# Kernel tuning notes

Measured on AMD Instinct MI355X. Metric: run time of the kernel, lower is better.

Reference implementation:

```python
import jax, jax.numpy as jnp
import numpy as np

D = 64
NEG = 0.01            # leakyrelu_neg_slope
X_CONN = 0.25         # x_connection_init
SKIP_H = 0.5          # skip_weight_h
SIGMAS = np.asarray(1.5 ** np.arange(15), np.float32)  # all_sigmas_dist

N_LIG, N_REC = 4096, 8192
E_LIG, E_REC = 65536, 262144
F_LIG, F_REC, NRBF = 15, 27, 15


def _lrelu(x):
    return jax.nn.leaky_relu(x, NEG)


def _ln(x, g, b, eps=1e-5):
    m = x.mean(-1, keepdims=True)
    v = ((x - m) ** 2).mean(-1, keepdims=True)
    return (x - m) * jax.lax.rsqrt(v + eps) * g + b


def _mlp2(x, w1, b1, g, bt, w2, b2):
    # nn.Sequential(Linear, Dropout(0), LeakyReLU, LayerNorm, Linear) in eval mode
    return _ln(_lrelu(x @ w1 + b1), g, bt) @ w2 + b2


def _coords_mlp(m, w1, b1, w2, b2):
    # nn.Sequential(Linear, Dropout(0), LeakyReLU, Linear(out,1))
    return _lrelu(m @ w1 + b1) @ w2 + b2  # [E, 1]


def _seg_mean(v, idx, n):
    # DGL fn.mean over incoming edges at destination nodes (0 for isolated nodes)
    s = jax.ops.segment_sum(v, idx, num_segments=n)
    c = jax.ops.segment_sum(jnp.ones(idx.shape, v.dtype), idx, num_segments=n)
    return s / jnp.maximum(c, 1.0)[:, None]


def setup_inputs() -> dict:
    key = jax.random.key(0)
    ks = iter(jax.random.split(key, 64))

    def n(shape, s=1.0):
        return jax.random.normal(next(ks), shape, jnp.float32) * s

    def lin(i, o):
        return n((i, o), 1.0 / float(np.sqrt(i)))

    zeros = lambda *s: jnp.zeros(s, jnp.float32)
    ones = lambda *s: jnp.ones(s, jnp.float32)

    d = {}
    d['coords_lig'] = n((N_LIG, 3))
    d['h_lig'] = n((N_LIG, D))
    d['orig_h_lig'] = n((N_LIG, D))
    d['orig_coords_lig'] = n((N_LIG, 3))
    d['coords_rec'] = n((N_REC, 3))
    d['h_rec'] = n((N_REC, D))
    d['orig_h_rec'] = n((N_REC, D))
    d['orig_coords_rec'] = n((N_REC, 3))
    d['lig_src'] = jax.random.randint(next(ks), (E_LIG,), 0, N_LIG)
    d['lig_dst'] = jax.random.randint(next(ks), (E_LIG,), 0, N_LIG)
    d['lig_efeat'] = n((E_LIG, F_LIG))
    d['rec_src'] = jax.random.randint(next(ks), (E_REC,), 0, N_REC)
    d['rec_dst'] = jax.random.randint(next(ks), (E_REC,), 0, N_REC)
    d['rec_efeat'] = n((E_REC, F_REC))
    d['mask'] = (jax.random.uniform(next(ks), (N_LIG, N_REC)) < 0.5).astype(jnp.float32)
    # ---- parameters ----
    d['lig_em_w1'], d['lig_em_b1'] = lin(2 * D + F_LIG + NRBF, D), zeros(D)
    d['lig_em_g'], d['lig_em_bt'] = ones(D), zeros(D)
    d['lig_em_w2'], d['lig_em_b2'] = lin(D, D), zeros(D)
    d['rec_em_w1'], d['rec_em_b1'] = lin(2 * D + F_REC + NRBF, D), zeros(D)
    d['rec_em_g'], d['rec_em_bt'] = ones(D), zeros(D)
    d['rec_em_w2'], d['rec_em_b2'] = lin(D, D), zeros(D)
    d['lig_cm_w1'], d['lig_cm_b1'] = lin(D, D), zeros(D)
    d['lig_cm_w2'], d['lig_cm_b2'] = lin(D, 1), zeros(1)
    d['rec_cm_w1'], d['rec_cm_b1'] = lin(D, D), zeros(D)
    d['rec_cm_w2'], d['rec_cm_b2'] = lin(D, 1), zeros(1)
    for nm in ['q_lig_w', 'k_lig_w', 'v_lig_w', 'q_rec_w', 'k_rec_w', 'v_rec_w']:
        d[nm] = lin(D, D)
    d['lig_nm_w1'], d['lig_nm_b1'] = lin(4 * D, D), zeros(D)
    d['lig_nm_g'], d['lig_nm_bt'] = ones(D), zeros(D)
    d['lig_nm_w2'], d['lig_nm_b2'] = lin(D, D), zeros(D)
    d['rec_nm_w1'], d['rec_nm_b1'] = lin(4 * D, D), zeros(D)
    d['rec_nm_g'], d['rec_nm_bt'] = ones(D), zeros(D)
    d['rec_nm_w2'], d['rec_nm_b2'] = lin(D, D), zeros(D)
    return d


def reference(coords_lig, h_lig, orig_h_lig, orig_coords_lig,
              coords_rec, h_rec, orig_h_rec, orig_coords_rec,
              lig_src, lig_dst, lig_efeat, rec_src, rec_dst, rec_efeat, mask,
              lig_em_w1, lig_em_b1, lig_em_g, lig_em_bt, lig_em_w2, lig_em_b2,
              rec_em_w1, rec_em_b1, rec_em_g, rec_em_bt, rec_em_w2, rec_em_b2,
              lig_cm_w1, lig_cm_b1, lig_cm_w2, lig_cm_b2,
              rec_cm_w1, rec_cm_b1, rec_cm_w2, rec_cm_b2,
              q_lig_w, k_lig_w, v_lig_w, q_rec_w, k_rec_w, v_rec_w,
              lig_nm_w1, lig_nm_b1, lig_nm_g, lig_nm_bt, lig_nm_w2, lig_nm_b2,
              rec_nm_w1, rec_nm_b1, rec_nm_g, rec_nm_bt, rec_nm_w2, rec_nm_b2):
    n_lig, n_rec = coords_lig.shape[0], coords_rec.shape[0]
    sig = jnp.asarray(SIGMAS, coords_lig.dtype)

    # --- ligand edge messages: x_rel = x_src - x_dst, multi-scale RBF of |x_rel|^2 ---
    xr_l = coords_lig[lig_src] - coords_lig[lig_dst]                       # [E_l, 3]
    rbf_l = jnp.exp(-jnp.sum(xr_l * xr_l, -1, keepdims=True) / sig)        # [E_l, 15]
    msg_l = _mlp2(jnp.concatenate([h_lig[lig_src], h_lig[lig_dst], lig_efeat, rbf_l], -1),
                  lig_em_w1, lig_em_b1, lig_em_g, lig_em_bt, lig_em_w2, lig_em_b2)

    # --- receptor edge messages (rec_square_distance_scale = 1) ---
    xr_r = coords_rec[rec_src] - coords_rec[rec_dst]
    rbf_r = jnp.exp(-jnp.sum(xr_r * xr_r, -1, keepdims=True) / sig)
    msg_r = _mlp2(jnp.concatenate([h_rec[rec_src], h_rec[rec_dst], rec_efeat, rbf_r], -1),
                  rec_em_w1, rec_em_b1, rec_em_g, rec_em_bt, rec_em_w2, rec_em_b2)

    # --- masked cross-graph attention (pre/post cross-msg norms are identity) ---
    q_l, k_l, v_l = _lrelu(h_lig @ q_lig_w), _lrelu(h_lig @ k_lig_w), h_lig @ v_lig_w
    q_r, k_r, v_r = _lrelu(h_rec @ q_rec_w), _lrelu(h_rec @ k_rec_w), h_rec @ v_rec_w
    s_lr = mask * (q_l @ k_r.T) - 1000.0 * (1.0 - mask)
    att_l = jax.nn.softmax(s_lr, axis=1) @ v_r                             # [N_l, D]
    mt = mask.T
    s_rl = mt * (q_r @ k_l.T) - 1000.0 * (1.0 - mt)
    att_r = jax.nn.softmax(s_rl, axis=1) @ v_l                             # [N_r, D]

    # --- equivariant coordinate update: mean_j phi_x(m_ij) * x_rel, + skip to orig ---
    coef_l = _coords_mlp(msg_l, lig_cm_w1, lig_cm_b1, lig_cm_w2, lig_cm_b2)
    x_lig = X_CONN * orig_coords_lig + (1.0 - X_CONN) * coords_lig + _seg_mean(xr_l * coef_l, lig_dst, n_lig)
    coef_r = _coords_mlp(msg_r, rec_cm_w1, rec_cm_b1, rec_cm_w2, rec_cm_b2)
    x_rec = X_CONN * orig_coords_rec + (1.0 - X_CONN) * coords_rec + _seg_mean(xr_r * coef_r, rec_dst, n_rec)

    # --- node feature update with skip (h_feats_dim == out_feats_dim) ---
    aggr_l = _seg_mean(msg_l, lig_dst, n_lig)
    h_lig_out = SKIP_H * _mlp2(jnp.concatenate([h_lig, aggr_l, att_l, orig_h_lig], -1),
                               lig_nm_w1, lig_nm_b1, lig_nm_g, lig_nm_bt, lig_nm_w2, lig_nm_b2) \
        + (1.0 - SKIP_H) * h_lig
    aggr_r = _seg_mean(msg_r, rec_dst, n_rec)
    h_rec_out = SKIP_H * _mlp2(jnp.concatenate([h_rec, aggr_r, att_r, orig_h_rec], -1),
                               rec_nm_w1, rec_nm_b1, rec_nm_g, rec_nm_bt, rec_nm_w2, rec_nm_b2) \
        + (1.0 - SKIP_H) * h_rec
    return x_lig, h_lig_out, x_rec, h_rec_out
```

## Files before the change

### kernel.cpp

```cpp
#include <hip/hip_runtime.h>
#include <hip/hip_bf16.h>

typedef __hip_bfloat16 bf16;
typedef __attribute__((ext_vector_type(8))) short bfrag8;
typedef __attribute__((ext_vector_type(4))) float f32x4;

#define N_LIG 4096
#define N_REC 8192
#define E_LIG 65536
#define E_REC 262144
#define F_LIGc 15
#define F_RECc 27

__device__ __forceinline__ float ldkv(const float* p, size_t i) { return p[i]; }
__device__ __forceinline__ float ldkv(const bf16* p, size_t i) { return __bfloat162float(p[i]); }
__device__ __forceinline__ short bfbits(float x) {
    bf16 b = __float2bfloat16(x);
    return *(short*)&b;
}
__device__ __forceinline__ unsigned short stg(const float* p, size_t i) {
    return (unsigned short)bfbits(p[i]);
}
__device__ __forceinline__ unsigned short stg(const bf16* p, size_t i) {
    return *(const unsigned short*)(p + i);
}
__device__ __forceinline__ void stage16(unsigned short* d, const bf16* s) {
    *(uint4*)d = *(const uint4*)s;
}
__device__ __forceinline__ void stage16(unsigned short* d, const float* s) {
    float4 a = *(const float4*)s;
    float4 b = *(const float4*)(s + 4);
    unsigned short tmp[8] = {
        (unsigned short)bfbits(a.x), (unsigned short)bfbits(a.y),
        (unsigned short)bfbits(a.z), (unsigned short)bfbits(a.w),
        (unsigned short)bfbits(b.x), (unsigned short)bfbits(b.y),
        (unsigned short)bfbits(b.z), (unsigned short)bfbits(b.w)};
    *(uint4*)d = *(uint4*)tmp;
}

__device__ __forceinline__ int swz(int row, int col) {
    return (row << 6) + ((((col >> 3) ^ row ^ (row >> 3)) & 7) << 3) + (col & 7);
}

__constant__ float c_inv_sigma[15] = {
    1.0f, 0.6666666667f, 0.4444444444f, 0.2962962963f, 0.1975308642f,
    0.1316872428f, 0.08779149520f, 0.05852766346f, 0.03901844231f,
    0.02601229487f, 0.01734152992f, 0.01156101994f, 0.007707346628f,
    0.005138231085f, 0.003425487390f};

__device__ __forceinline__ float wave_sum(float v) {
    #pragma unroll
    for (int o = 32; o > 0; o >>= 1) v += __shfl_xor(v, o, 64);
    return v;
}
__device__ __forceinline__ float quad_max(float v) {
    v = fmaxf(v, __shfl_xor(v, 1)); v = fmaxf(v, __shfl_xor(v, 2));
    v = fmaxf(v, __shfl_xor(v, 4)); v = fmaxf(v, __shfl_xor(v, 8));
    return v;
}

__device__ __forceinline__ void pack_body(
    int b, int t,
    const float* w_rec1, const float* w_lig1, const float* w_rec2, const float* w_lig2,
    const float* c_rec1, const float* c_lig1,
    unsigned short* p_rec1, unsigned short* p_lig1,
    unsigned short* p_rec2, unsigned short* p_lig2,
    unsigned short* pc_rec1, unsigned short* pc_lig1)
{
    const float* src; unsigned short* dst; int kk, IN;
    if (b < 6)       { src = w_rec1; dst = p_rec1;  kk = b;      IN = 170; }
    else if (b < 11) { src = w_lig1; dst = p_lig1;  kk = b - 6;  IN = 158; }
    else if (b < 13) { src = w_rec2; dst = p_rec2;  kk = b - 11; IN = 64; }
    else if (b < 15) { src = w_lig2; dst = p_lig2;  kk = b - 13; IN = 64; }
    else if (b < 17) { src = c_rec1; dst = pc_rec1; kk = b - 15; IN = 64; }
    else             { src = c_lig1; dst = pc_lig1; kk = b - 17; IN = 64; }
    int wv = t >> 6, L = t & 63, lm = L & 15, qd = L >> 4;
    int n = wv * 16 + lm;
    unsigned short tmp[8];
    #pragma unroll
    for (int j = 0; j < 8; ++j) {
        int k = kk * 32 + qd * 8 + j;
        tmp[j] = (k < IN) ? (unsigned short)bfbits(src[k * 64 + n]) : (unsigned short)0;
    }
    *(uint4*)&dst[((size_t)(kk * 4 + wv) * 64 + L) * 8] = *(uint4*)tmp;
}

__device__ __forceinline__ void kv_body(
    int job, int j,
    const float* h_lig, const float* h_rec,
    const float* kwl, const float* vwl, const float* kwr, const float* vwr,
    bf16* kbl, bf16* vbl, bf16* kbr, bf16* vbr)
{
    const float *h, *w; bf16* out; int node, do_l;
    if (job < N_LIG)                  { h = h_lig; w = kwl; out = kbl; node = job;                     do_l = 1; }
    else if (job < 2 * N_LIG)         { h = h_lig; w = vwl; out = vbl; node = job - N_LIG;             do_l = 0; }
    else if (job < 2 * N_LIG + N_REC) { h = h_rec; w = kwr; out = kbr; node = job - 2 * N_LIG;         do_l = 1; }
    else                              { h = h_rec; w = vwr; out = vbr; node = job - 2 * N_LIG - N_REC; do_l = 0; }
    float xv = h[(size_t)node * 64 + j];
    float acc = 0.f;
    #pragma unroll
    for (int i = 0; i < 64; ++i) acc += __shfl(xv, i, 64) * w[i * 64 + j];
    if (do_l) acc = acc > 0.f ? acc : 0.01f * acc;
    out[(size_t)node * 64 + j] = __float2bfloat16(acc);
}

__device__ __forceinline__ void mask_body(
    unsigned char* tr, unsigned char* tc, int bx, int by, int t,
    const float* mask, unsigned long long* mq, unsigned long long* mqT, int R, int C)
{
    int r0 = by * 64, c0 = bx * 64;
    int cs = (t & 15) * 4;
    #pragma unroll
    for (int rr = 0; rr < 4; ++rr) {
        int r = (t >> 4) + rr * 16;
        const float* mp = &mask[(size_t)(r0 + r) * C + c0 + cs];
        unsigned char b0 = mp[0] != 0.f, b1 = mp[1] != 0.f;
        unsigned char b2 = mp[2] != 0.f, b3 = mp[3] != 0.f;
        tr[r * 68 + cs + 0] = b0; tr[r * 68 + cs + 1] = b1;
        tr[r * 68 + cs + 2] = b2; tr[r * 68 + cs + 3] = b3;
        tc[(cs + 0) * 68 + r] = b0; tc[(cs + 1) * 68 + r] = b1;
        tc[(cs + 2) * 68 + r] = b2; tc[(cs + 3) * 68 + r] = b3;
    }
    __syncthreads();
    if (t < 128) {
        const unsigned* p = (t < 64) ? (const unsigned*)&tr[t * 68]
                                     : (const unsigned*)&tc[(t - 64) * 68];
        unsigned lo = 0, hi = 0;
        #pragma unroll
        for (int i = 0; i < 8; ++i)
            lo |= (((p[i] & 0x01010101u) * 0x01020408u) >> 24 & 0xFu) << (4 * i);
        #pragma unroll
        for (int i = 8; i < 16; ++i)
            hi |= (((p[i] & 0x01010101u) * 0x01020408u) >> 24 & 0xFu) << (4 * (i - 8));
        unsigned long long w = (unsigned long long)lo | ((unsigned long long)hi << 32);
        if (t < 64) mq[(size_t)(c0 >> 6) * R + r0 + t] = w;
        else        mqT[(size_t)(r0 >> 6) * C + c0 + (t - 64)] = w;
    }
}

#define NB_MASK  ((N_REC / 64) * (N_LIG / 64))
#define N_CVT    (N_LIG * 64 + N_REC * 64 + E_LIG * F_LIGc + E_REC * F_RECc)
#define NB_CVT   (N_CVT / 256)
#define NB_KV    (2 * (N_LIG + N_REC) / 4)
#define N_ZERO   (N_LIG * 64 + N_REC * 64 + N_LIG * 3 + N_REC * 3 + N_LIG + N_REC)
#define NB_HIST  ((E_LIG + E_REC) / 256)
#define NB_PACK  19
#define NB_PREP  (NB_MASK + NB_CVT + NB_KV + NB_HIST + NB_PACK)

__global__ __launch_bounds__(256) void prep_kernel(
    const float* __restrict__ mask, unsigned long long* __restrict__ mq,
    unsigned long long* __restrict__ mqT,
    const float* __restrict__ h_lig, bf16* __restrict__ hb_l,
    const float* __restrict__ h_rec, bf16* __restrict__ hb_r,
    const float* __restrict__ ef_l, bf16* __restrict__ efb_l,
    const float* __restrict__ ef_r, bf16* __restrict__ efb_r,
    const float* __restrict__ kwl, const float* __restrict__ vwl,
    const float* __restrict__ kwr, const float* __restrict__ vwr,
    bf16* __restrict__ kbl, bf16* __restrict__ vbl,
    bf16* __restrict__ kbr, bf16* __restrict__ vbr,
    const int* __restrict__ dl, const int* __restrict__ dr,
    int* __restrict__ cl, int* __restrict__ cr,
    const float* w_rec1, const float* w_lig1, const float* w_rec2, const float* w_lig2,
    const float* c_rec1, const float* c_lig1,
    unsigned short* p_rec1, unsigned short* p_lig1,
    unsigned short* p_rec2, unsigned short* p_lig2,
    unsigned short* pc_rec1, unsigned short* pc_lig1)
{
    __shared__ unsigned char tr[64 * 68];
    __shared__ unsigned char tc[64 * 68];
    int b = blockIdx.x, t = threadIdx.x;
    if (b < NB_MASK) {
        mask_body(tr, tc, b & 127, b >> 7, t, mask, mq, mqT, N_LIG, N_REC);
        return;
    }
    b -= NB_MASK;
    if (b < NB_CVT) {
        int i = b * 256 + t;
        if (i < N_LIG * 64) { hb_l[i] = __float2bfloat16(h_lig[i]); return; }
        i -= N_LIG * 64;
        if (i < N_REC * 64) { hb_r[i] = __float2bfloat16(h_rec[i]); return; }
        i -= N_REC * 64;
        if (i < E_LIG * F_LIGc) { efb_l[i] = __float2bfloat16(ef_l[i]); return; }
        i -= E_LIG * F_LIGc;
        efb_r[i] = __float2bfloat16(ef_r[i]);
        return;
    }
    b -= NB_CVT;
    if (b < NB_KV) {
        kv_body(b * 4 + (t >> 6), t & 63, h_lig, h_rec, kwl, vwl, kwr, vwr,
                kbl, vbl, kbr, vbr);
        return;
    }
    b -= NB_KV;
    if (b < NB_HIST) {
        int i = b * 256 + t;
        if (i < E_LIG) atomicAdd(&cl[dl[i]], 1);
        else atomicAdd(&cr[dr[i - E_LIG]], 1);
        return;
    }
    b -= NB_HIST;
    pack_body(b, t, w_rec1, w_lig1, w_rec2, w_lig2, c_rec1, c_lig1,
              p_rec1, p_lig1, p_rec2, p_lig2, pc_rec1, pc_lig1);
}

__global__ void zero_kernel(float* __restrict__ p, int n) {
    int i = blockIdx.x * blockDim.x + threadIdx.x;
    if (i < n) p[i] = 0.f;
}
__global__ void hist2_kernel(const int* __restrict__ dl, const int* __restrict__ dr,
                             int* __restrict__ cl, int* __restrict__ cr) {
    int i = blockIdx.x * 256 + threadIdx.x;
    if (i < E_LIG) { atomicAdd(&cl[dl[i]], 1); return; }
    i -= E_LIG;
    if (i < E_REC) atomicAdd(&cr[dr[i]], 1);
}
__global__ __launch_bounds__(256) void pack_frags(
    const float* w_rec1, const float* w_lig1, const float* w_rec2, const float* w_lig2,
    const float* c_rec1, const float* c_lig1,
    unsigned short* p_rec1, unsigned short* p_lig1,
    unsigned short* p_rec2, unsigned short* p_lig2,
    unsigned short* pc_rec1, unsigned short* pc_lig1)
{
    pack_body(blockIdx.x, threadIdx.x, w_rec1, w_lig1, w_rec2, w_lig2, c_rec1, c_lig1,
              p_rec1, p_lig1, p_rec2, p_lig2, pc_rec1, pc_lig1);
}
__global__ __launch_bounds__(256) void kv_proj_kernel(
    const float* __restrict__ h_lig, const float* __restrict__ h_rec,
    const float* __restrict__ kwl, const float* __restrict__ vwl,
    const float* __restrict__ kwr, const float* __restrict__ vwr,
    bf16* __restrict__ kbl, bf16* __restrict__ vbl,
    bf16* __restrict__ kbr, bf16* __restrict__ vbr)
{
    kv_body(blockIdx.x * 4 + (threadIdx.x >> 6), threadIdx.x & 63,
            h_lig, h_rec, kwl, vwl, kwr, vwr, kbl, vbl, kbr, vbr);
}

__global__ __launch_bounds__(256) void scan2_kernel(
    const int* __restrict__ cl, int* __restrict__ curl,
    const int* __restrict__ cr, int* __restrict__ curr)
{
    const int* counts = blockIdx.x ? cr : cl;
    int* cursor = blockIdx.x ? curr : curl;
    int n = blockIdx.x ? N_REC : N_LIG;
    __shared__ int part[256];
    int t = threadIdx.x;
    int c = n / 256;
    int base = t * c;
    int s = 0;
    for (int i = 0; i < c; ++i) s += counts[base + i];
    part[t] = s;
    __syncthreads();
    for (int o = 1; o < 256; o <<= 1) {
        int u = (t >= o) ? part[t - o] : 0;
        __syncthreads();
        part[t] += u;
        __syncthreads();
    }
    int run = part[t] - s;
    for (int i = 0; i < c; ++i) {
        cursor[base + i] = run;
        run += counts[base + i];
    }
}

__global__ void scatter2_kernel(const int* __restrict__ dl, const int* __restrict__ dr,
                                int* __restrict__ curl, int* __restrict__ curr,
                                int* __restrict__ ordl, int* __restrict__ ordr) {
    int i = blockIdx.x * 256 + threadIdx.x;
    if (i < E_LIG) { ordl[atomicAdd(&curl[dl[i]], 1)] = i; return; }
    i -= E_LIG;
    if (i < E_REC) ordr[atomicAdd(&curr[dr[i]], 1)] = i;
}

template <int F, int K1S, typename HT>
__device__ __forceinline__ void edge_body(
    char* sbuf, int ebid,
    const int* __restrict__ order,
    const float* __restrict__ coords, const HT* __restrict__ h,
    const int* __restrict__ src, const int* __restrict__ dst,
    const HT* __restrict__ efeat,
    const unsigned short* __restrict__ w1p, const float* __restrict__ b1,
    const float* __restrict__ g, const float* __restrict__ bt,
    const unsigned short* __restrict__ w2p, const float* __restrict__ b2,
    const unsigned short* __restrict__ c1p, const float* __restrict__ cb1,
    const float* __restrict__ cw2, const float* __restrict__ cb2,
    float* __restrict__ aggr, float* __restrict__ xacc)
{
    constexpr int IN = 143 + F;
    constexpr int KP = K1S * 32 + 8;
    constexpr int XB = 64 * KP * 2;
    static_assert(XB >= 64 * 68 * 4, "msgf f32 alias must fit in xb");
    static_assert(XB >= 64 * 72 * 2, "h1b alias must fit in xb");
    unsigned short* xb   = (unsigned short*)sbuf;
    unsigned short* h1b  = (unsigned short*)sbuf;
    float*          msgf = (float*)sbuf;
    float* wsum1   = (float*)(sbuf + XB);
    float* wsum2   = (float*)(sbuf + XB + 1024);
    float* stat_m  = (float*)(sbuf + XB + 2048);
    float* stat_r  = (float*)(sbuf + XB + 2304);
    float* coefp   = (float*)(sbuf + XB + 2560);
    float* coef_all= (float*)(sbuf + XB + 3584);
    int*   srcs    = (int*)(sbuf + XB + 3840);
    int*   dsts    = (int*)(sbuf + XB + 4096);
    int*   ords    = (int*)(sbuf + XB + 4352);
    float* xr_s    = (float*)(sbuf + XB + 4608);
    float* d2s     = (float*)(sbuf + XB + 5376);

// ... 406 lines not shown
        #pragma unroll
        for (int r = 0; r < 4; ++r) {
            int row = r0 + wv * 16 + qd * 4 + r;
            pM[(size_t)sp * n_rows + row] = rm[r];
            pL[(size_t)sp * n_rows + row] = osum[r];
        }
    }
}

__global__ __launch_bounds__(256, 4) void mega_kernel(
    int nb1,
    const float* h1, const float* qw1, const bf16* k1, const bf16* v1,
    const unsigned long long* mq1, float* pO1, float* pM1, float* pL1,
    int nrows1, int ncols1, int ns1,
    const float* h2, const float* qw2, const bf16* k2, const bf16* v2,
    const unsigned long long* mq2, float* pO2, float* pM2, float* pL2,
    int nrows2, int ncols2, int ns2,
    const int* ordR, const float* coordsR, const bf16* hR,
    const int* srcR, const int* dstR, const bf16* efR,
    const unsigned short* w1pR, const float* b1R, const float* gR, const float* btR,
    const unsigned short* w2pR, const float* b2R,
    const unsigned short* c1pR, const float* cb1R, const float* cw2R, const float* cb2R,
    float* aggrR, float* xaccR,
    const int* ordL, const float* coordsL, const bf16* hL,
    const int* srcL, const int* dstL, const bf16* efL,
    const unsigned short* w1pL, const float* b1L, const float* gL, const float* btL,
    const unsigned short* w2pL, const float* b2L,
    const unsigned short* c1pL, const float* cb1L, const float* cw2L, const float* cb2L,
    float* aggrL, float* xaccL)
{
    __shared__ __align__(16) char sbuf[31232];
    int bid = blockIdx.x;
    const int nbAtt = (N_LIG / 64) * ns1 + (N_REC / 64) * ns2;
    if (bid < nbAtt) {
        attn_body<0>(sbuf, bid, nb1,
            h1, qw1, k1, v1, mq1, (const float*)0, 0L, 0L, pO1, pM1, pL1, nrows1, ncols1, ns1,
            h2, qw2, k2, v2, mq2, (const float*)0, 0L, 0L, pO2, pM2, pL2, nrows2, ncols2, ns2);
    } else {
        int eid = bid - nbAtt;
        if (eid < E_REC / 64)
            edge_body<F_RECc, 6, bf16>(sbuf, eid, ordR, coordsR, hR, srcR, dstR, efR,
                w1pR, b1R, gR, btR, w2pR, b2R, c1pR, cb1R, cw2R, cb2R, aggrR, xaccR);
        else
            edge_body<F_LIGc, 5, bf16>(sbuf, eid - E_REC / 64, ordL, coordsL, hL, srcL, dstL, efL,
                w1pL, b1L, gL, btL, w2pL, b2L, c1pL, cb1L, cw2L, cb2L, aggrL, xaccL);
    }
}

template <int F, int K1S>
__global__ __launch_bounds__(256, 4) void edge_mfma_f(
    const int* order, const float* coords, const float* h,
    const int* src, const int* dst, const float* efeat,
    const unsigned short* w1p, const float* b1, const float* g, const float* bt,
    const unsigned short* w2p, const float* b2,
    const unsigned short* c1p, const float* cb1, const float* cw2, const float* cb2,
    float* aggr, float* xacc)
{
    __shared__ __align__(16) char sbuf[64 * (K1S * 32 + 8) * 2 + 5632];
    edge_body<F, K1S, float>(sbuf, blockIdx.x, order, coords, h, src, dst, efeat,
        w1p, b1, g, bt, w2p, b2, c1p, cb1, cw2, cb2, aggr, xacc);
}

__global__ __launch_bounds__(256, 4) void attn_f32mask(
    int nb1,
    const float* h1, const float* qw1, const bf16* k1, const bf16* v1,
    const float* mf1, long mrs1, long mcs1,
    float* pO1, float* pM1, float* pL1, int nrows1, int ncols1, int ns1,
    const float* h2, const float* qw2, const bf16* k2, const bf16* v2,
    const float* mf2, long mrs2, long mcs2,
    float* pO2, float* pM2, float* pL2, int nrows2, int ncols2, int ns2)
{
    __shared__ __align__(16) char sbuf[29696];
    attn_body<1>(sbuf, blockIdx.x, nb1,
        h1, qw1, k1, v1, (const unsigned long long*)0, mf1, mrs1, mcs1,
        pO1, pM1, pL1, nrows1, ncols1, ns1,
        h2, qw2, k2, v2, (const unsigned long long*)0, mf2, mrs2, mcs2,
        pO2, pM2, pL2, nrows2, ncols2, ns2);
}

__global__ __launch_bounds__(256, 3) void node_mfma(
    int nbl, int nbn,
    const float* h1, const float* __restrict__ aggr1, const int* __restrict__ cnt1,
    const float* att1, const float* __restrict__ origh1,
    const float* __restrict__ w1a, const float* __restrict__ b1a,
    const float* __restrict__ ga, const float* __restrict__ bta,
    const float* __restrict__ w2a, const float* __restrict__ b2a, float* out1,
    const float* h2, const float* __restrict__ aggr2, const int* __restrict__ cnt2,
    const float* att2, const float* __restrict__ origh2,
    const float* __restrict__ w1b, const float* __restrict__ b1b,
    const float* __restrict__ gb, const float* __restrict__ btb,
    const float* __restrict__ w2b, const float* __restrict__ b2b, float* out2,
    const float* __restrict__ ocl, const float* __restrict__ ccl,
    const float* __restrict__ xaccl, float* __restrict__ outxl,
    const float* __restrict__ ocr, const float* __restrict__ ccr,
    const float* __restrict__ xaccr, float* __restrict__ outxr)
{
    if ((int)blockIdx.x >= nbn) {
        int i = (blockIdx.x - nbn) * 256 + threadIdx.x;
        if (i < N_LIG * 3) {
            int node = i / 3;
            float invc = 1.f / fmaxf((float)cnt1[node], 1.f);
            outxl[i] = 0.25f * ocl[i] + 0.75f * ccl[i] + xaccl[i] * invc;
        } else {
            i -= N_LIG * 3;
            if (i < N_REC * 3) {
                int node = i / 3;
                float invc = 1.f / fmaxf((float)cnt2[node], 1.f);
                outxr[i] = 0.25f * ocr[i] + 0.75f * ccr[i] + xaccr[i] * invc;
            }
        }
        return;
    }

    const float *h, *aggr, *att, *orig_h, *w1, *b1, *g, *bt, *w2, *b2;
    const int* cnt;
    float* h_out;
    int n0;
    if ((int)blockIdx.x < nbl) {
        h = h1; aggr = aggr1; cnt = cnt1; att = att1; orig_h = origh1;
        w1 = w1a; b1 = b1a; g = ga; bt = bta; w2 = w2a; b2 = b2a; h_out = out1;
        n0 = blockIdx.x * 64;
    } else {
        h = h2; aggr = aggr2; cnt = cnt2; att = att2; orig_h = origh2;
        w1 = w1b; b1 = b1b; g = gb; bt = btb; w2 = w2b; b2 = b2b; h_out = out2;
        n0 = (blockIdx.x - nbl) * 64;
    }

    constexpr int KP = 264;
    __shared__ __align__(16) char smem[64 * KP * 2];
    __shared__ __align__(16) unsigned short h1b[64 * 72];
    __shared__ float sums[256], sums2[256];
    __shared__ float stat_m[64], stat_r[64];
    unsigned short* xb  = (unsigned short*)smem;
    float*          h1f = (float*)smem;

    const int t  = threadIdx.x;
    const int lm = t & 15;
    const int qd = (t & 63) >> 4;
    const int n  = (t >> 6) * 16 + lm;

    bfrag8 w1f[8], w2f[2];
    #pragma unroll
    for (int kk = 0; kk < 8; ++kk)
        #pragma unroll
        for (int j = 0; j < 8; ++j) {
            int k = kk * 32 + qd * 8 + j;
            w1f[kk][j] = bfbits(w1[k * 64 + n]);
        }
    #pragma unroll
    for (int kk = 0; kk < 2; ++kk)
        #pragma unroll
        for (int j = 0; j < 8; ++j) {
            int k = kk * 32 + qd * 8 + j;
            w2f[kk][j] = bfbits(w2[k * 64 + n]);
        }
    const float b1n = b1[n], b2n = b2[n];

    for (int p = 0; p < 16; ++p) {
        int e = (t >> 6) + 4 * p;
        int node = n0 + e;
        float invc = 1.f / fmaxf((float)cnt[node], 1.f);
        int j = t & 63;
        xb[e * KP + j]       = bfbits(h[(size_t)node * 64 + j]);
        xb[e * KP + 64 + j]  = bfbits(aggr[(size_t)node * 64 + j] * invc);
        xb[e * KP + 128 + j] = bfbits(att[(size_t)node * 64 + j]);
        xb[e * KP + 192 + j] = bfbits(orig_h[(size_t)node * 64 + j]);
    }
    __syncthreads();

    f32x4 acc1[4];
    #pragma unroll
    for (int m = 0; m < 4; ++m) {
        f32x4 acc = {0.f, 0.f, 0.f, 0.f};
        #pragma unroll
        for (int kk = 0; kk < 8; ++kk) {
            bfrag8 a = *(const bfrag8*)&xb[(m * 16 + lm) * KP + kk * 32 + qd * 8];
            acc = __builtin_amdgcn_mfma_f32_16x16x32_bf16(a, w1f[kk], acc, 0, 0, 0);
        }
        acc1[m] = acc;
    }
    __syncthreads();
    #pragma unroll
    for (int m = 0; m < 4; ++m)
        #pragma unroll
        for (int r = 0; r < 4; ++r) {
            int mr = m * 16 + qd * 4 + r;
            float v = acc1[m][r] + b1n;
            v = v > 0.f ? v : 0.01f * v;
            h1f[mr * 68 + n] = v;
        }
    __syncthreads();

    {
        int e = t >> 2, seg = (t & 3) * 16;
        float s1 = 0.f, s2 = 0.f;
        #pragma unroll
        for (int j = 0; j < 16; ++j) {
            float v = h1f[e * 68 + seg + j];
            s1 += v; s2 += v * v;
        }
        sums[t] = s1; sums2[t] = s2;
    }
    __syncthreads();
    if (t < 64) {
        float s1 = sums[4 * t] + sums[4 * t + 1] + sums[4 * t + 2] + sums[4 * t + 3];
        float s2 = sums2[4 * t] + sums2[4 * t + 1] + sums2[4 * t + 2] + sums2[4 * t + 3];
        float mean = s1 * (1.f / 64.f);
        float var = s2 * (1.f / 64.f) - mean * mean;
        stat_m[t] = mean;
        stat_r[t] = rsqrtf(fmaxf(var, 0.f) + 1e-5f);
    }
    __syncthreads();
    for (int idx = t; idx < 4096; idx += 256) {
        int e = idx >> 6, j = idx & 63;
        float v = (h1f[e * 68 + j] - stat_m[e]) * stat_r[e] * g[j] + bt[j];
        h1b[e * 72 + j] = bfbits(v);
    }
    __syncthreads();

    #pragma unroll
    for (int m = 0; m < 4; ++m) {
        f32x4 acc = {0.f, 0.f, 0.f, 0.f};
        #pragma unroll
        for (int kk = 0; kk < 2; ++kk) {
            bfrag8 a = *(const bfrag8*)&h1b[(m * 16 + lm) * 72 + kk * 32 + qd * 8];
            acc = __builtin_amdgcn_mfma_f32_16x16x32_bf16(a, w2f[kk], acc, 0, 0, 0);
        }
        #pragma unroll
        for (int r = 0; r < 4; ++r) {
            int row = n0 + m * 16 + qd * 4 + r;
            float o = acc[r] + b2n;
            float hv = h[(size_t)row * 64 + n];
            h_out[(size_t)row * 64 + n] = 0.5f * o + 0.5f * hv;
        }
    }
}

__global__ __launch_bounds__(64) void attn_merge2(
    const float* __restrict__ pO1, const float* __restrict__ pM1, const float* __restrict__ pL1,
    float* __restrict__ out1, int ns1,
    const float* __restrict__ pO2, const float* __restrict__ pM2, const float* __restrict__ pL2,
    float* __restrict__ out2, int ns2)
{
    int r = blockIdx.x;
    const float *pO, *pM, *pL; float* out; int n_rows, nsplit;
    if (r < N_LIG) { pO = pO1; pM = pM1; pL = pL1; out = out1; n_rows = N_LIG; nsplit = ns1; }
    else { r -= N_LIG; pO = pO2; pM = pM2; pL = pL2; out = out2; n_rows = N_REC; nsplit = ns2; }
    int d = threadIdx.x;
    float mstar = -1e30f;
// ... 47 lines not shown
    int wid = tid >> 6;
    if ((tid & 63) == 0) red[wid] = lmax;
    __syncthreads();
    float bmax = fmaxf(fmaxf(red[0], red[1]), fmaxf(red[2], red[3]));
    __syncthreads();

    float lsum = 0.f;
    for (int c = tid; c < n_cols; c += 256) {
        float e = __expf(sc[c] - bmax);
        sc[c] = e;
        lsum += e;
    }
    lsum = wave_sum(lsum);
    if ((tid & 63) == 0) red[wid] = lsum;
    __syncthreads();
    float inv = 1.f / (red[0] + red[1] + red[2] + red[3]);

    int dd = tid & 63;
    float o = 0.f;
    for (int c = wid; c < n_cols; c += 4) o += sc[c] * ldkv(v, (size_t)c * 64 + dd);
    opart[wid][dd] = o;
    __syncthreads();
    if (wid == 0)
        out[(size_t)row * 64 + dd] =
            (opart[0][dd] + opart[1][dd] + opart[2][dd] + opart[3][dd]) * inv;
}

extern "C" void kernel_launch(void* const* d_in, const int* in_sizes, int n_in,
                              void* d_out, int out_size, void* d_ws, size_t ws_size,
                              hipStream_t stream)
{
    const float* coords_lig      = (const float*)d_in[0];
    const float* h_lig           = (const float*)d_in[1];
    const float* orig_h_lig      = (const float*)d_in[2];
    const float* orig_coords_lig = (const float*)d_in[3];
    const float* coords_rec      = (const float*)d_in[4];
    const float* h_rec           = (const float*)d_in[5];
    const float* orig_h_rec      = (const float*)d_in[6];
    const float* orig_coords_rec = (const float*)d_in[7];
    const int* lig_src   = (const int*)d_in[8];
    const int* lig_dst   = (const int*)d_in[9];
    const float* lig_efeat = (const float*)d_in[10];
    const int* rec_src   = (const int*)d_in[11];
    const int* rec_dst   = (const int*)d_in[12];
    const float* rec_efeat = (const float*)d_in[13];
    const float* mask      = (const float*)d_in[14];
    const float *lig_em_w1 = (const float*)d_in[15], *lig_em_b1 = (const float*)d_in[16];
    const float *lig_em_g  = (const float*)d_in[17], *lig_em_bt = (const float*)d_in[18];
    const float *lig_em_w2 = (const float*)d_in[19], *lig_em_b2 = (const float*)d_in[20];
    const float *rec_em_w1 = (const float*)d_in[21], *rec_em_b1 = (const float*)d_in[22];
    const float *rec_em_g  = (const float*)d_in[23], *rec_em_bt = (const float*)d_in[24];
    const float *rec_em_w2 = (const float*)d_in[25], *rec_em_b2 = (const float*)d_in[26];
    const float *lig_cm_w1 = (const float*)d_in[27], *lig_cm_b1 = (const float*)d_in[28];
    const float *lig_cm_w2 = (const float*)d_in[29], *lig_cm_b2 = (const float*)d_in[30];
    const float *rec_cm_w1 = (const float*)d_in[31], *rec_cm_b1 = (const float*)d_in[32];
    const float *rec_cm_w2 = (const float*)d_in[33], *rec_cm_b2 = (const float*)d_in[34];
    const float *q_lig_w = (const float*)d_in[35], *k_lig_w = (const float*)d_in[36];
    const float *v_lig_w = (const float*)d_in[37], *q_rec_w = (const float*)d_in[38];
    const float *k_rec_w = (const float*)d_in[39], *v_rec_w = (const float*)d_in[40];
    const float *lig_nm_w1 = (const float*)d_in[41], *lig_nm_b1 = (const float*)d_in[42];
    const float *lig_nm_g  = (const float*)d_in[43], *lig_nm_bt = (const float*)d_in[44];
    const float *lig_nm_w2 = (const float*)d_in[45], *lig_nm_b2 = (const float*)d_in[46];
    const float *rec_nm_w1 = (const float*)d_in[47], *rec_nm_b1 = (const float*)d_in[48];
    const float *rec_nm_g  = (const float*)d_in[49], *rec_nm_bt = (const float*)d_in[50];
    const float *rec_nm_w2 = (const float*)d_in[51], *rec_nm_b2 = (const float*)d_in[52];

    char* wsb = (char*)d_ws;
    float* aggr_l = (float*)(wsb + 16);
    float* aggr_r = aggr_l + (size_t)N_LIG * 64;
    float* xacc_l = aggr_r + (size_t)N_REC * 64;
    float* xacc_r = xacc_l + (size_t)N_LIG * 3;
    int* counts_l = (int*)(xacc_r + (size_t)N_REC * 3);
    int* counts_r = counts_l + N_LIG;
    int* cursor_l = counts_r + N_REC;
    int* cursor_r = cursor_l + N_LIG;
    int* order_l  = cursor_r + N_REC;
    int* order_r  = order_l + E_LIG;
    unsigned short* p_rec1  = (unsigned short*)(order_r + E_REC);
    unsigned short* p_lig1  = p_rec1 + 6 * 2048;
    unsigned short* p_rec2  = p_lig1 + 5 * 2048;
    unsigned short* p_lig2  = p_rec2 + 2 * 2048;
    unsigned short* pc_rec1 = p_lig2 + 2 * 2048;
    unsigned short* pc_lig1 = pc_rec1 + 2 * 2048;
    char* kv_base = (char*)(pc_lig1 + 2 * 2048);
    const size_t core_b = (size_t)(kv_base - wsb);
    const size_t kv_b = (size_t)(N_LIG + N_REC) * 64 * 2 * 2;

    const size_t mq1_n = (size_t)(N_REC / 64) * N_LIG;
    const size_t mq2_n = (size_t)(N_LIG / 64) * N_REC;
    const size_t mq_all_b = (mq1_n + mq2_n) * 8;
    const size_t mir_b = (size_t)(N_LIG + N_REC) * 64 * 2
                       + ((size_t)E_LIG * F_LIGc + (size_t)E_REC * F_RECc) * 2;

    const size_t part_b_hi = ((size_t)16 * N_LIG * 64 + (size_t)8 * N_REC * 64) * 4
                           + ((size_t)16 * N_LIG + (size_t)8 * N_REC) * 2 * 4;
    const size_t part_b_lo = ((size_t)4 * N_LIG * 64 + (size_t)2 * N_REC * 64) * 4
                           + ((size_t)4 * N_LIG + (size_t)2 * N_REC) * 2 * 4;

    int tier, ns1, ns2;
    size_t part_b;
    if (ws_size >= core_b + kv_b + part_b_hi + mq_all_b + mir_b) {
        tier = 0; ns1 = 16; ns2 = 8; part_b = part_b_hi;
    } else if (ws_size >= core_b + kv_b + part_b_lo) {
        tier = 1; ns1 = 4; ns2 = 2; part_b = part_b_lo;
    } else {
        tier = 2; ns1 = 4; ns2 = 2; part_b = part_b_lo;
    }

    bf16* kb_l = (bf16*)kv_base;
    bf16* vb_l = kb_l + (size_t)N_LIG * 64;
    bf16* kb_r = vb_l + (size_t)N_LIG * 64;
    bf16* vb_r = kb_r + (size_t)N_REC * 64;
    float* pO1 = (float*)(kv_base + kv_b);
    float* pO2 = pO1 + (size_t)ns1 * N_LIG * 64;
    float* pM1 = pO2 + (size_t)ns2 * N_REC * 64;
    float* pL1 = pM1 + (size_t)ns1 * N_LIG;
    float* pM2 = pL1 + (size_t)ns1 * N_LIG;
    float* pL2 = pM2 + (size_t)ns2 * N_REC;
    unsigned long long* mqb  = (unsigned long long*)(kv_base + kv_b + part_b);
    unsigned long long* mqbT = mqb + mq1_n;
    bf16* hb_l  = (bf16*)(mqbT + mq2_n);
    bf16* hb_r  = hb_l + (size_t)N_LIG * 64;
    bf16* efb_l = hb_r + (size_t)N_REC * 64;
    bf16* efb_r = efb_l + (size_t)E_LIG * F_LIGc;

    float* out = (float*)d_out;
    float* x_lig_o = out;
    float* h_lig_o = out + 12288;
    float* x_rec_o = out + 274432;
    float* h_rec_o = out + 299008;

    const int nb1 = (N_LIG / 64) * ns1;
    const int nb2 = (N_REC / 64) * ns2;

    if (tier == 0) {
        zero_kernel<<<(N_ZERO + 255) / 256, 256, 0, stream>>>(aggr_l, N_ZERO);
        prep_kernel<<<NB_PREP, 256, 0, stream>>>(
            mask, mqb, mqbT,
            h_lig, hb_l, h_rec, hb_r, lig_efeat, efb_l, rec_efeat, efb_r,
            k_lig_w, v_lig_w, k_rec_w, v_rec_w, kb_l, vb_l, kb_r, vb_r,
            lig_dst, rec_dst, counts_l, counts_r,
            rec_em_w1, lig_em_w1, rec_em_w2, lig_em_w2, rec_cm_w1, lig_cm_w1,
            p_rec1, p_lig1, p_rec2, p_lig2, pc_rec1, pc_lig1);
        scan2_kernel<<<2, 256, 0, stream>>>(counts_l, cursor_l, counts_r, cursor_r);
        scatter2_kernel<<<(E_LIG + E_REC) / 256, 256, 0, stream>>>(
            lig_dst, rec_dst, cursor_l, cursor_r, order_l, order_r);

        mega_kernel<<<nb1 + nb2 + (E_LIG + E_REC) / 64, 256, 0, stream>>>(
            nb1,
            h_lig, q_lig_w, kb_r, vb_r, mqb, pO1, pM1, pL1, N_LIG, N_REC, ns1,
            h_rec, q_rec_w, kb_l, vb_l, mqbT, pO2, pM2, pL2, N_REC, N_LIG, ns2,
            order_r, coords_rec, hb_r, rec_src, rec_dst, efb_r,
            p_rec1, rec_em_b1, rec_em_g, rec_em_bt, p_rec2, rec_em_b2,
            pc_rec1, rec_cm_b1, rec_cm_w2, rec_cm_b2, aggr_r, xacc_r,
            order_l, coords_lig, hb_l, lig_src, lig_dst, efb_l,
            p_lig1, lig_em_b1, lig_em_g, lig_em_bt, p_lig2, lig_em_b2,
            pc_lig1, lig_cm_b1, lig_cm_w2, lig_cm_b2, aggr_l, xacc_l);

        attn_merge2<<<N_LIG + N_REC, 64, 0, stream>>>(
            pO1, pM1, pL1, h_lig_o, ns1, pO2, pM2, pL2, h_rec_o, ns2);
    } else {
        zero_kernel<<<(N_ZERO + 255) / 256, 256, 0, stream>>>(aggr_l, N_ZERO);
        pack_frags<<<19, 256, 0, stream>>>(
            rec_em_w1, lig_em_w1, rec_em_w2, lig_em_w2, rec_cm_w1, lig_cm_w1,
            p_rec1, p_lig1, p_rec2, p_lig2, pc_rec1, pc_lig1);
        hist2_kernel<<<(E_LIG + E_REC) / 256, 256, 0, stream>>>(
            lig_dst, rec_dst, counts_l, counts_r);
        scan2_kernel<<<2, 256, 0, stream>>>(counts_l, cursor_l, counts_r, cursor_r);
        scatter2_kernel<<<(E_LIG + E_REC) / 256, 256, 0, stream>>>(
            lig_dst, rec_dst, cursor_l, cursor_r, order_l, order_r);
        kv_proj_kernel<<<(2 * (N_LIG + N_REC)) / 4, 256, 0, stream>>>(
            h_lig, h_rec, k_lig_w, v_lig_w, k_rec_w, v_rec_w,
            kb_l, vb_l, kb_r, vb_r);

        edge_mfma_f<F_LIGc, 5><<<E_LIG / 64, 256, 0, stream>>>(
            order_l, coords_lig, h_lig, lig_src, lig_dst, lig_efeat,
            p_lig1, lig_em_b1, lig_em_g, lig_em_bt, p_lig2, lig_em_b2,
            pc_lig1, lig_cm_b1, lig_cm_w2, lig_cm_b2, aggr_l, xacc_l);
        edge_mfma_f<F_RECc, 6><<<E_REC / 64, 256, 0, stream>>>(
            order_r, coords_rec, h_rec, rec_src, rec_dst, rec_efeat,
            p_rec1, rec_em_b1, rec_em_g, rec_em_bt, p_rec2, rec_em_b2,
            pc_rec1, rec_cm_b1, rec_cm_w2, rec_cm_b2, aggr_r, xacc_r);
        if (tier == 1) {
            attn_f32mask<<<nb1 + nb2, 256, 0, stream>>>(
                nb1,
                h_lig, q_lig_w, kb_r, vb_r, mask, (long)N_REC, 1L,
                pO1, pM1, pL1, N_LIG, N_REC, ns1,
                h_rec, q_rec_w, kb_l, vb_l, mask, 1L, (long)N_REC,
                pO2, pM2, pL2, N_REC, N_LIG, ns2);
            attn_merge2<<<N_LIG + N_REC, 64, 0, stream>>>(
                pO1, pM1, pL1, h_lig_o, ns1, pO2, pM2, pL2, h_rec_o, ns2);
        } else {
            attn_row_kernel<<<N_LIG, 256, N_REC * sizeof(float), stream>>>(
                h_lig, q_lig_w, kb_r, vb_r, mask, (long)N_REC, 1L, h_lig_o, N_REC);
            attn_row_kernel<<<N_REC, 256, N_LIG * sizeof(float), stream>>>(
                h_rec, q_rec_w, kb_l, vb_l, mask, 1L, (long)N_REC, h_rec_o, N_LIG);
        }
    }

    const int nbn = N_LIG / 64 + N_REC / 64;
    const int nbc = ((N_LIG + N_REC) * 3 + 255) / 256;
    node_mfma<<<nbn + nbc, 256, 0, stream>>>(
        N_LIG / 64, nbn,
        h_lig, aggr_l, counts_l, h_lig_o, orig_h_lig,
        lig_nm_w1, lig_nm_b1, lig_nm_g, lig_nm_bt, lig_nm_w2, lig_nm_b2, h_lig_o,
        h_rec, aggr_r, counts_r, h_rec_o, orig_h_rec,
        rec_nm_w1, rec_nm_b1, rec_nm_g, rec_nm_bt, rec_nm_w2, rec_nm_b2, h_rec_o,
        orig_coords_lig, coords_lig, xacc_l, x_lig_o,
        orig_coords_rec, coords_rec, xacc_r, x_rec_o);
}
```

Baseline: 571.5 us.

## Prepack node-MLP weights, vectorize bf16 conversion, fold zeroing into prep kernel

Node-MLP weights are now packed once into MFMA fragment layout in the prep and pack kernels, so node_mfma blocks load fragments with single vector loads instead of gathering scalar fp32 weights in every block. Node-feature staging in node_mfma uses float4 loads with the per-node inverse count held in shared memory. The fp32-to-bf16 conversion handles four elements per thread, and most buffer zeroing moves into prep_kernel blocks so the standalone zero kernel only clears the counts. In exchange the prep launch grows, and the pack stage gains blocks and workspace.

```diff
diff --git a/kernel.cpp b/kernel.cpp
--- a/kernel.cpp
+++ b/kernel.cpp
@@ -37,6 +37,13 @@
         (unsigned short)bfbits(b.z), (unsigned short)bfbits(b.w)};
     *(uint4*)d = *(uint4*)tmp;
 }
+__device__ __forceinline__ void cv4(bf16* d, const float* s) {
+    float4 v = *(const float4*)s;
+    unsigned short tmp[4] = {
+        (unsigned short)bfbits(v.x), (unsigned short)bfbits(v.y),
+        (unsigned short)bfbits(v.z), (unsigned short)bfbits(v.w)};
+    *(uint2*)d = *(uint2*)tmp;
+}
 
 __device__ __forceinline__ int swz(int row, int col) {
     return (row << 6) + ((((col >> 3) ^ row ^ (row >> 3)) & 7) << 3) + (col & 7);
@@ -63,9 +70,12 @@
     int b, int t,
     const float* w_rec1, const float* w_lig1, const float* w_rec2, const float* w_lig2,
     const float* c_rec1, const float* c_lig1,
+    const float* n_rec1, const float* n_lig1, const float* n_rec2, const float* n_lig2,
     unsigned short* p_rec1, unsigned short* p_lig1,
     unsigned short* p_rec2, unsigned short* p_lig2,
-    unsigned short* pc_rec1, unsigned short* pc_lig1)
+    unsigned short* pc_rec1, unsigned short* pc_lig1,
+    unsigned short* pn_rec1, unsigned short* pn_lig1,
+    unsigned short* pn_rec2, unsigned short* pn_lig2)
 {
     const float* src; unsigned short* dst; int kk, IN;
     if (b < 6)       { src = w_rec1; dst = p_rec1;  kk = b;      IN = 170; }
@@ -73,7 +83,11 @@
     else if (b < 13) { src = w_rec2; dst = p_rec2;  kk = b - 11; IN = 64; }
     else if (b < 15) { src = w_lig2; dst = p_lig2;  kk = b - 13; IN = 64; }
     else if (b < 17) { src = c_rec1; dst = pc_rec1; kk = b - 15; IN = 64; }
-    else             { src = c_lig1; dst = pc_lig1; kk = b - 17; IN = 64; }
+    else if (b < 19) { src = c_lig1; dst = pc_lig1; kk = b - 17; IN = 64; }
+    else if (b < 27) { src = n_rec1; dst = pn_rec1; kk = b - 19; IN = 256; }
+    else if (b < 35) { src = n_lig1; dst = pn_lig1; kk = b - 27; IN = 256; }
+    else if (b < 37) { src = n_rec2; dst = pn_rec2; kk = b - 35; IN = 64; }
+    else             { src = n_lig2; dst = pn_lig2; kk = b - 37; IN = 64; }
     int wv = t >> 6, L = t & 63, lm = L & 15, qd = L >> 4;
     int n = wv * 16 + lm;
     unsigned short tmp[8];
@@ -138,14 +152,16 @@
     }
 }
 
-#define NB_MASK  ((N_REC / 64) * (N_LIG / 64))
-#define N_CVT    (N_LIG * 64 + N_REC * 64 + E_LIG * F_LIGc + E_REC * F_RECc)
-#define NB_CVT   (N_CVT / 256)
-#define NB_KV    (2 * (N_LIG + N_REC) / 4)
-#define N_ZERO   (N_LIG * 64 + N_REC * 64 + N_LIG * 3 + N_REC * 3 + N_LIG + N_REC)
-#define NB_HIST  ((E_LIG + E_REC) / 256)
-#define NB_PACK  19
-#define NB_PREP  (NB_MASK + NB_CVT + NB_KV + NB_HIST + NB_PACK)
+#define NB_MASK   ((N_REC / 64) * (N_LIG / 64))
+#define N_CVT     (N_LIG * 64 + N_REC * 64 + E_LIG * F_LIGc + E_REC * F_RECc)
+#define NB_CVT4   (N_CVT / 1024)
+#define NB_KV     (2 * (N_LIG + N_REC) / 4)
+#define N_ZEROA   (N_LIG * 64 + N_REC * 64 + N_LIG * 3 + N_REC * 3)
+#define NB_ZEROA  (N_ZEROA / 256)
+#define N_ZERO    (N_ZEROA + N_LIG + N_REC)
+#define NB_HIST   ((E_LIG + E_REC) / 256)
+#define NB_PACK   39
+#define NB_PREP   (NB_MASK + NB_CVT4 + NB_KV + NB_ZEROA + NB_HIST + NB_PACK)
 
 __global__ __launch_bounds__(256) void prep_kernel(
     const float* __restrict__ mask, unsigned long long* __restrict__ mq,
@@ -158,13 +174,17 @@
     const float* __restrict__ kwr, const float* __restrict__ vwr,
     bf16* __restrict__ kbl, bf16* __restrict__ vbl,
     bf16* __restrict__ kbr, bf16* __restrict__ vbr,
+    float* __restrict__ zp,
     const int* __restrict__ dl, const int* __restrict__ dr,
     int* __restrict__ cl, int* __restrict__ cr,
     const float* w_rec1, const float* w_lig1, const float* w_rec2, const float* w_lig2,
     const float* c_rec1, const float* c_lig1,
+    const float* n_rec1, const float* n_lig1, const float* n_rec2, const float* n_lig2,
     unsigned short* p_rec1, unsigned short* p_lig1,
     unsigned short* p_rec2, unsigned short* p_lig2,
-    unsigned short* pc_rec1, unsigned short* pc_lig1)
+    unsigned short* pc_rec1, unsigned short* pc_lig1,
+    unsigned short* pn_rec1, unsigned short* pn_lig1,
+    unsigned short* pn_rec2, unsigned short* pn_lig2)
 {
     __shared__ unsigned char tr[64 * 68];
     __shared__ unsigned char tc[64 * 68];
@@ -174,24 +194,29 @@
         return;
     }
     b -= NB_MASK;
-    if (b < NB_CVT) {
-        int i = b * 256 + t;
-        if (i < N_LIG * 64) { hb_l[i] = __float2bfloat16(h_lig[i]); return; }
+    if (b < NB_CVT4) {
+        int i = (b * 256 + t) * 4;
+        if (i < N_LIG * 64) { cv4(hb_l + i, h_lig + i); return; }
         i -= N_LIG * 64;
-        if (i < N_REC * 64) { hb_r[i] = __float2bfloat16(h_rec[i]); return; }
+        if (i < N_REC * 64) { cv4(hb_r + i, h_rec + i); return; }
         i -= N_REC * 64;
-        if (i < E_LIG * F_LIGc) { efb_l[i] = __float2bfloat16(ef_l[i]); return; }
+        if (i < E_LIG * F_LIGc) { cv4(efb_l + i, ef_l + i); return; }
         i -= E_LIG * F_LIGc;
-        efb_r[i] = __float2bfloat16(ef_r[i]);
+        cv4(efb_r + i, ef_r + i);
         return;
     }
-    b -= NB_CVT;
+    b -= NB_CVT4;
     if (b < NB_KV) {
         kv_body(b * 4 + (t >> 6), t & 63, h_lig, h_rec, kwl, vwl, kwr, vwr,
                 kbl, vbl, kbr, vbr);
         return;
     }
     b -= NB_KV;
+    if (b < NB_ZEROA) {
+        zp[b * 256 + t] = 0.f;
+        return;
+    }
+    b -= NB_ZEROA;
     if (b < NB_HIST) {
         int i = b * 256 + t;
         if (i < E_LIG) atomicAdd(&cl[dl[i]], 1);
@@ -200,7 +225,9 @@
     }
     b -= NB_HIST;
     pack_body(b, t, w_rec1, w_lig1, w_rec2, w_lig2, c_rec1, c_lig1,
-              p_rec1, p_lig1, p_rec2, p_lig2, pc_rec1, pc_lig1);
+              n_rec1, n_lig1, n_rec2, n_lig2,
+              p_rec1, p_lig1, p_rec2, p_lig2, pc_rec1, pc_lig1,
+              pn_rec1, pn_lig1, pn_rec2, pn_lig2);
 }
 
 __global__ void zero_kernel(float* __restrict__ p, int n) {
@@ -217,12 +244,17 @@
 __global__ __launch_bounds__(256) void pack_frags(
     const float* w_rec1, const float* w_lig1, const float* w_rec2, const float* w_lig2,
     const float* c_rec1, const float* c_lig1,
+    const float* n_rec1, const float* n_lig1, const float* n_rec2, const float* n_lig2,
     unsigned short* p_rec1, unsigned short* p_lig1,
     unsigned short* p_rec2, unsigned short* p_lig2,
-    unsigned short* pc_rec1, unsigned short* pc_lig1)
+    unsigned short* pc_rec1, unsigned short* pc_lig1,
+    unsigned short* pn_rec1, unsigned short* pn_lig1,
+    unsigned short* pn_rec2, unsigned short* pn_lig2)
 {
     pack_body(blockIdx.x, threadIdx.x, w_rec1, w_lig1, w_rec2, w_lig2, c_rec1, c_lig1,
-              p_rec1, p_lig1, p_rec2, p_lig2, pc_rec1, pc_lig1);
+              n_rec1, n_lig1, n_rec2, n_lig2,
+              p_rec1, p_lig1, p_rec2, p_lig2, pc_rec1, pc_lig1,
+              pn_rec1, pn_lig1, pn_rec2, pn_lig2);
 }
 __global__ __launch_bounds__(256) void kv_proj_kernel(
     const float* __restrict__ h_lig, const float* __restrict__ h_rec,
@@ -795,14 +827,14 @@
     int nbl, int nbn,
     const float* h1, const float* __restrict__ aggr1, const int* __restrict__ cnt1,
     const float* att1, const float* __restrict__ origh1,
-    const float* __restrict__ w1a, const float* __restrict__ b1a,
+    const unsigned short* __restrict__ w1pa, const float* __restrict__ b1a,
     const float* __restrict__ ga, const float* __restrict__ bta,
-    const float* __restrict__ w2a, const float* __restrict__ b2a, float* out1,
+    const unsigned short* __restrict__ w2pa, const float* __restrict__ b2a, float* out1,
     const float* h2, const float* __restrict__ aggr2, const int* __restrict__ cnt2,
     const float* att2, const float* __restrict__ origh2,
-    const float* __restrict__ w1b, const float* __restrict__ b1b,
+    const unsigned short* __restrict__ w1pb, const float* __restrict__ b1b,
     const float* __restrict__ gb, const float* __restrict__ btb,
-    const float* __restrict__ w2b, const float* __restrict__ b2b, float* out2,
+    const unsigned short* __restrict__ w2pb, const float* __restrict__ b2b, float* out2,
     const float* __restrict__ ocl, const float* __restrict__ ccl,
     const float* __restrict__ xaccl, float* __restrict__ outxl,
     const float* __restrict__ ocr, const float* __restrict__ ccr,
@@ -825,17 +857,18 @@
         return;
     }
 
-    const float *h, *aggr, *att, *orig_h, *w1, *b1, *g, *bt, *w2, *b2;
+    const float *h, *aggr, *att, *orig_h, *b1, *g, *bt, *b2;
+    const unsigned short *w1p, *w2p;
     const int* cnt;
     float* h_out;
     int n0;
     if ((int)blockIdx.x < nbl) {
         h = h1; aggr = aggr1; cnt = cnt1; att = att1; orig_h = origh1;
-        w1 = w1a; b1 = b1a; g = ga; bt = bta; w2 = w2a; b2 = b2a; h_out = out1;
+        w1p = w1pa; b1 = b1a; g = ga; bt = bta; w2p = w2pa; b2 = b2a; h_out = out1;
         n0 = blockIdx.x * 64;
     } else {
         h = h2; aggr = aggr2; cnt = cnt2; att = att2; orig_h = origh2;
-        w1 = w1b; b1 = b1b; g = gb; bt = btb; w2 = w2b; b2 = b2b; h_out = out2;
+        w1p = w1pb; b1 = b1b; g = gb; bt = btb; w2p = w2pb; b2 = b2b; h_out = out2;
         n0 = (blockIdx.x - nbl) * 64;
     }
 
@@ -844,40 +877,49 @@
     __shared__ __align__(16) unsigned short h1b[64 * 72];
     __shared__ float sums[256], sums2[256];
     __shared__ float stat_m[64], stat_r[64];
+    __shared__ float invc_s[64];
     unsigned short* xb  = (unsigned short*)smem;
     float*          h1f = (float*)smem;
 
     const int t  = threadIdx.x;
+    const int wv = t >> 6;
+    const int L  = t & 63;
     const int lm = t & 15;
     const int qd = (t & 63) >> 4;
-    const int n  = (t >> 6) * 16 + lm;
+    const int n  = wv * 16 + lm;
 
     bfrag8 w1f[8], w2f[2];
     #pragma unroll
     for (int kk = 0; kk < 8; ++kk)
-        #pragma unroll
-        for (int j = 0; j < 8; ++j) {
-            int k = kk * 32 + qd * 8 + j;
-            w1f[kk][j] = bfbits(w1[k * 64 + n]);
-        }
+        w1f[kk] = *(const bfrag8*)&w1p[((size_t)(kk * 4 + wv) * 64 + L) * 8];
     #pragma unroll
     for (int kk = 0; kk < 2; ++kk)
-        #pragma unroll
-        for (int j = 0; j < 8; ++j) {
-            int k = kk * 32 + qd * 8 + j;
-            w2f[kk][j] = bfbits(w2[k * 64 + n]);
-        }
+        w2f[kk] = *(const bfrag8*)&w2p[((size_t)(kk * 4 + wv) * 64 + L) * 8];
     const float b1n = b1[n], b2n = b2[n];
 
-    for (int p = 0; p < 16; ++p) {
-        int e = (t >> 6) + 4 * p;
-        int node = n0 + e;
-        float invc = 1.f / fmaxf((float)cnt[node], 1.f);
-        int j = t & 63;
-        xb[e * KP + j]       = bfbits(h[(size_t)node * 64 + j]);
-        xb[e * KP + 64 + j]  = bfbits(aggr[(size_t)node * 64 + j] * invc);
-        xb[e * KP + 128 + j] = bfbits(att[(size_t)node * 64 + j]);
-        xb[e * KP + 192 + j] = bfbits(orig_h[(size_t)node * 64 + j]);
+    if (t < 64) invc_s[t] = 1.f / fmaxf((float)cnt[n0 + t], 1.f);
+    __syncthreads();
+
+    #pragma unroll
+    for (int it = 0; it < 8; ++it) {
+        int idx = t + 256 * it;
+        int e   = idx >> 5;
+        int c   = idx & 31;
+        int arr = c >> 3, ch = (c & 7) * 8;
+        const float* sp;
+        if      (arr == 0) sp = h      + (size_t)(n0 + e) * 64 + ch;
+        else if (arr == 1) sp = aggr   + (size_t)(n0 + e) * 64 + ch;
+        else if (arr == 2) sp = att    + (size_t)(n0 + e) * 64 + ch;
+        else               sp = orig_h + (size_t)(n0 + e) * 64 + ch;
+        float4 a = *(const float4*)sp;
+        float4 b = *(const float4*)(sp + 4);
+        float s = (arr == 1) ? invc_s[e] : 1.f;
+        unsigned short tmp[8] = {
+            (unsigned short)bfbits(a.x * s), (unsigned short)bfbits(a.y * s),
+            (unsigned short)bfbits(a.z * s), (unsigned short)bfbits(a.w * s),
+            (unsigned short)bfbits(b.x * s), (unsigned short)bfbits(b.y * s),
+            (unsigned short)bfbits(b.z * s), (unsigned short)bfbits(b.w * s)};
+        *(uint4*)&xb[e * KP + arr * 64 + ch] = *(uint4*)tmp;
     }
     __syncthreads();
 
@@ -1091,7 +1133,11 @@
     unsigned short* p_lig2  = p_rec2 + 2 * 2048;
     unsigned short* pc_rec1 = p_lig2 + 2 * 2048;
     unsigned short* pc_lig1 = pc_rec1 + 2 * 2048;
-    char* kv_base = (char*)(pc_lig1 + 2 * 2048);
+    unsigned short* pn_rec1 = pc_lig1 + 2 * 2048;
+    unsigned short* pn_lig1 = pn_rec1 + 8 * 2048;
+    unsigned short* pn_rec2 = pn_lig1 + 8 * 2048;
+    unsigned short* pn_lig2 = pn_rec2 + 2 * 2048;
+    char* kv_base = (char*)(pn_lig2 + 2 * 2048);
     const size_t core_b = (size_t)(kv_base - wsb);
     const size_t kv_b = (size_t)(N_LIG + N_REC) * 64 * 2 * 2;
 
@@ -1143,14 +1189,18 @@
     const int nb2 = (N_REC / 64) * ns2;
 
     if (tier == 0) {
-        zero_kernel<<<(N_ZERO + 255) / 256, 256, 0, stream>>>(aggr_l, N_ZERO);
+        zero_kernel<<<(N_LIG + N_REC + 255) / 256, 256, 0, stream>>>(
+            (float*)counts_l, N_LIG + N_REC);
         prep_kernel<<<NB_PREP, 256, 0, stream>>>(
             mask, mqb, mqbT,
             h_lig, hb_l, h_rec, hb_r, lig_efeat, efb_l, rec_efeat, efb_r,
             k_lig_w, v_lig_w, k_rec_w, v_rec_w, kb_l, vb_l, kb_r, vb_r,
+            aggr_l,
             lig_dst, rec_dst, counts_l, counts_r,
             rec_em_w1, lig_em_w1, rec_em_w2, lig_em_w2, rec_cm_w1, lig_cm_w1,
-            p_rec1, p_lig1, p_rec2, p_lig2, pc_rec1, pc_lig1);
+            rec_nm_w1, lig_nm_w1, rec_nm_w2, lig_nm_w2,
+            p_rec1, p_lig1, p_rec2, p_lig2, pc_rec1, pc_lig1,
+            pn_rec1, pn_lig1, pn_rec2, pn_lig2);
         scan2_kernel<<<2, 256, 0, stream>>>(counts_l, cursor_l, counts_r, cursor_r);
         scatter2_kernel<<<(E_LIG + E_REC) / 256, 256, 0, stream>>>(
             lig_dst, rec_dst, cursor_l, cursor_r, order_l, order_r);
@@ -1170,9 +1220,11 @@
             pO1, pM1, pL1, h_lig_o, ns1, pO2, pM2, pL2, h_rec_o, ns2);
     } else {
         zero_kernel<<<(N_ZERO + 255) / 256, 256, 0, stream>>>(aggr_l, N_ZERO);
-        pack_frags<<<19, 256, 0, stream>>>(
+        pack_frags<<<NB_PACK, 256, 0, stream>>>(
             rec_em_w1, lig_em_w1, rec_em_w2, lig_em_w2, rec_cm_w1, lig_cm_w1,
-            p_rec1, p_lig1, p_rec2, p_lig2, pc_rec1, pc_lig1);
+            rec_nm_w1, lig_nm_w1, rec_nm_w2, lig_nm_w2,
+            p_rec1, p_lig1, p_rec2, p_lig2, pc_rec1, pc_lig1,
+            pn_rec1, pn_lig1, pn_rec2, pn_lig2);
         hist2_kernel<<<(E_LIG + E_REC) / 256, 256, 0, stream>>>(
             lig_dst, rec_dst, counts_l, counts_r);
         scan2_kernel<<<2, 256, 0, stream>>>(counts_l, cursor_l, counts_r, cursor_r);
@@ -1212,9 +1264,9 @@
     node_mfma<<<nbn + nbc, 256, 0, stream>>>(
         N_LIG / 64, nbn,
         h_lig, aggr_l, counts_l, h_lig_o, orig_h_lig,
-        lig_nm_w1, lig_nm_b1, lig_nm_g, lig_nm_bt, lig_nm_w2, lig_nm_b2, h_lig_o,
+        pn_lig1, lig_nm_b1, lig_nm_g, lig_nm_bt, pn_lig2, lig_nm_b2, h_lig_o,
         h_rec, aggr_r, counts_r, h_rec_o, orig_h_rec,
-        rec_nm_w1, rec_nm_b1, rec_nm_g, rec_nm_bt, rec_nm_w2, rec_nm_b2, h_rec_o,
+        pn_rec1, rec_nm_b1, rec_nm_g, rec_nm_bt, pn_rec2, rec_nm_b2, h_rec_o,
         orig_coords_lig, coords_lig, xacc_l, x_lig_o,
         orig_coords_rec, coords_rec, xacc_r, x_rec_o);
 }
```

After: 558.3 us. -2.3%, faster.
